# Optimization experiments

Hardware: AMD Instinct MI355X
Metric: run time of the kernel (lower is better)

Reference implementation:

```python
import jax, jax.numpy as jnp
import numpy as np

B, O, GRID = 2048, 48, 112
SIGMA = 5.0


def setup_inputs() -> dict:
    key = jax.random.key(0)
    k1, k2, k3, k4, k5 = jax.random.split(key, 5)
    s = float(GRID - 1)
    xL = jax.random.uniform(k1, (B,), dtype=jnp.float32) * s
    yL = jax.random.uniform(k2, (B,), dtype=jnp.float32) * s
    obj_list = jax.random.uniform(k3, (B, O, 2), dtype=jnp.float32) * s
    obj_num = jax.random.randint(k4, (B,), 0, O + 1, dtype=jnp.int32)
    road_mask = jax.random.randint(k5, (B, GRID, GRID), 0, 2, dtype=jnp.int32)
    return {"xL": xL, "yL": yL, "obj_list": obj_list, "obj_num": obj_num,
            "road_mask": road_mask, "H": GRID, "W": GRID}


def reference(xL, yL, obj_list, obj_num, road_mask, H, W):
    # Faithful vectorization of batch_gaussian_tensor_obj.
    # exp(-(dx^2+dy^2)/(2s^2)) is separable: exp(-dx^2/..) * exp(-dy^2/..),
    # so per-object splats reduce to a batched matmul over the object axis.
    inv = 1.0 / (2.0 * SIGMA * SIGMA)
    x = jnp.arange(H, dtype=jnp.float32)  # row coordinate grid
    y = jnp.arange(W, dtype=jnp.float32)  # col coordinate grid

    # positive goal gaussian, rank-1 outer product per batch element
    gx = jnp.exp(-((x[None, :] - xL[:, None]) ** 2) * inv)  # [B,H]
    gy = jnp.exp(-((y[None, :] - yL[:, None]) ** 2) * inv)  # [B,W]
    goal = gx[:, :, None] * gy[:, None, :]                   # [B,H,W]

    # negative object gaussians; note original swaps xy: xo=xy[1], yo=xy[0]
    xo = obj_list[:, :, 1]  # [B,O] row coords
    yo = obj_list[:, :, 0]  # [B,O] col coords
    ex = jnp.exp(-((x[None, None, :] - xo[:, :, None]) ** 2) * inv)  # [B,O,H]
    ey = jnp.exp(-((y[None, None, :] - yo[:, :, None]) ** 2) * inv)  # [B,O,W]
    valid = (jnp.arange(O)[None, :] < obj_num[:, None]).astype(jnp.float32)  # [B,O]
    obj = jnp.einsum('boh,bow->bhw', ex * valid[:, :, None], ey)     # [B,H,W]

    channel = 0.5 + 0.5 * goal - 0.5 * obj
    channel = jnp.where(road_mask == 0, 0.0, channel)
    return channel
```

## Files before the change

### kernel.cpp

```cpp
#include <hip/hip_runtime.h>

#define GRID_N 112
#define O_MAX 48
#define HW_N (GRID_N * GRID_N)
#define NT 256
#define KPAD 64
#define LSTR 72

typedef _Float16 half8  __attribute__((ext_vector_type(8)));
typedef _Float16 half2v __attribute__((ext_vector_type(2)));
typedef float    f32x4  __attribute__((ext_vector_type(4)));

__global__ __launch_bounds__(NT) void goalmap_kernel(
    const float* __restrict__ xL, const float* __restrict__ yL,
    const float* __restrict__ obj_list, const int* __restrict__ obj_num,
    const int* __restrict__ road_mask, float* __restrict__ out)
{
    constexpr float INV = 1.0f / (2.0f * 5.0f * 5.0f);

    __shared__ _Float16 exT[GRID_N * LSTR];
    __shared__ _Float16 eyT[GRID_N * LSTR];

    const int b   = blockIdx.x;
    const int tid = threadIdx.x;
    const int n   = obj_num[b];
    const float xl = xL[b];
    const float yl = yL[b];
    const float* ob = obj_list + (size_t)b * O_MAX * 2;

    for (int i = tid; i < GRID_N * (KPAD / 2); i += NT) {
        int pos = i >> 5;
        int o0  = (i & 31) * 2;
        half2v vx, vy;
        #pragma unroll
        for (int j = 0; j < 2; ++j) {
            int o = o0 + j;
            float valx = 0.f, valy = 0.f;
            if (o <= n) {
                float cx, cy, s;
                if (o < n) { cx = ob[o * 2 + 1]; cy = ob[o * 2 + 0]; s = -0.5f; }
                else       { cx = xl;            cy = yl;            s =  0.5f; }
                float dx = (float)pos - cx;
                float dy = (float)pos - cy;
                valx = s * __expf(-dx * dx * INV);
                valy =     __expf(-dy * dy * INV);
            }
            vx[j] = (_Float16)valx;
            vy[j] = (_Float16)valy;
        }
        *(half2v*)&exT[pos * LSTR + o0] = vx;
        *(half2v*)&eyT[pos * LSTR + o0] = vy;
    }
    __syncthreads();

    const int* rm = road_mask + (size_t)b * HW_N;
    float*     op = out       + (size_t)b * HW_N;

    const int lane = tid & 63;
    const int wid  = tid >> 6;
    const int m    = lane & 15;
    const int quad = lane >> 4;

    for (int t = wid; t < 49; t += 4) {
        int th = t / 7;
        int tw = t - th * 7;

        const _Float16* arow = &exT[(th * 16 + m) * LSTR + quad * 8];
        const _Float16* brow = &eyT[(tw * 16 + m) * LSTR + quad * 8];
        half8 a0 = *(const half8*)arow;
        half8 b0 = *(const half8*)brow;
        half8 a1 = *(const half8*)(arow + 32);
        half8 b1 = *(const half8*)(brow + 32);

        f32x4 acc = {0.f, 0.f, 0.f, 0.f};
        acc = __builtin_amdgcn_mfma_f32_16x16x32_f16(a0, b0, acc, 0, 0, 0);
        acc = __builtin_amdgcn_mfma_f32_16x16x32_f16(a1, b1, acc, 0, 0, 0);

        int h0 = th * 16 + quad * 4;
        int w0 = tw * 16 + m;
        #pragma unroll
        for (int r = 0; r < 4; ++r) {
            int idx = (h0 + r) * GRID_N + w0;
            int mv = rm[idx];
            float v = 0.5f + acc[r];
            op[idx] = (mv == 0) ? 0.f : v;
        }
    }
}

extern "C" void kernel_launch(void* const* d_in, const int* in_sizes, int n_in,
                              void* d_out, int out_size, void* d_ws, size_t ws_size,
                              hipStream_t stream) {
    const float* xL        = (const float*)d_in[0];
    const float* yL        = (const float*)d_in[1];
    const float* obj_list  = (const float*)d_in[2];
    const int*   obj_num   = (const int*)d_in[3];
    const int*   road_mask = (const int*)d_in[4];
    float*       out       = (float*)d_out;
    const int B = in_sizes[0];

    goalmap_kernel<<<B, NT, 0, stream>>>(xL, yL, obj_list, obj_num, road_mask, out);
}
```

Baseline: 219.6 us.

## Stage MFMA results in LDS and apply mask with vectorized 16-byte loads/stores

```diff
diff --git a/kernel.cpp b/kernel.cpp
--- a/kernel.cpp
+++ b/kernel.cpp
@@ -8,10 +8,11 @@
 #define LSTR 72
 
 typedef _Float16 half8  __attribute__((ext_vector_type(8)));
+typedef _Float16 half4v __attribute__((ext_vector_type(4)));
 typedef _Float16 half2v __attribute__((ext_vector_type(2)));
 typedef float    f32x4  __attribute__((ext_vector_type(4)));
 
-__global__ __launch_bounds__(NT) void goalmap_kernel(
+__global__ __launch_bounds__(NT, 2) void goalmap_kernel(
     const float* __restrict__ xL, const float* __restrict__ yL,
     const float* __restrict__ obj_list, const int* __restrict__ obj_num,
     const int* __restrict__ road_mask, float* __restrict__ out)
@@ -20,6 +21,7 @@
 
     __shared__ _Float16 exT[GRID_N * LSTR];
     __shared__ _Float16 eyT[GRID_N * LSTR];
+    __shared__ _Float16 cmap[HW_N];
 
     const int b   = blockIdx.x;
     const int tid = threadIdx.x;
@@ -53,9 +55,6 @@
     }
     __syncthreads();
 
-    const int* rm = road_mask + (size_t)b * HW_N;
-    float*     op = out       + (size_t)b * HW_N;
-
     const int lane = tid & 63;
     const int wid  = tid >> 6;
     const int m    = lane & 15;
@@ -79,12 +78,43 @@
         int h0 = th * 16 + quad * 4;
         int w0 = tw * 16 + m;
         #pragma unroll
-        for (int r = 0; r < 4; ++r) {
-            int idx = (h0 + r) * GRID_N + w0;
-            int mv = rm[idx];
-            float v = 0.5f + acc[r];
-            op[idx] = (mv == 0) ? 0.f : v;
+        for (int r = 0; r < 4; ++r)
+            cmap[(h0 + r) * GRID_N + w0] = (_Float16)(0.5f + acc[r]);
+    }
+    __syncthreads();
+
+    const int4*  rm4 = (const int4*)(road_mask + (size_t)b * HW_N);
+    float4*      op4 = (float4*)(out + (size_t)b * HW_N);
+
+    #pragma unroll
+    for (int it = 0; it < 3; ++it) {
+        int4   mv[4];
+        half4v cv[4];
+        #pragma unroll
+        for (int j = 0; j < 4; ++j) mv[j] = rm4[(it * 4 + j) * NT + tid];
+        #pragma unroll
+        for (int j = 0; j < 4; ++j)
+            cv[j] = *(const half4v*)&cmap[((it * 4 + j) * NT + tid) * 4];
+        #pragma unroll
+        for (int j = 0; j < 4; ++j) {
+            float4 v;
+            v.x = (mv[j].x == 0) ? 0.f : (float)cv[j][0];
+            v.y = (mv[j].y == 0) ? 0.f : (float)cv[j][1];
+            v.z = (mv[j].z == 0) ? 0.f : (float)cv[j][2];
+            v.w = (mv[j].w == 0) ? 0.f : (float)cv[j][3];
+            op4[(it * 4 + j) * NT + tid] = v;
         }
+    }
+    if (tid < 64) {
+        int idx = 12 * NT + tid;
+        int4   mv = rm4[idx];
+        half4v cv = *(const half4v*)&cmap[idx * 4];
+        float4 v;
+        v.x = (mv.x == 0) ? 0.f : (float)cv[0];
+        v.y = (mv.y == 0) ? 0.f : (float)cv[1];
+        v.z = (mv.z == 0) ? 0.f : (float)cv[2];
+        v.w = (mv.w == 0) ? 0.f : (float)cv[3];
+        op4[idx] = v;
     }
 }
 
```

After: 219.9 us. About the same (+0.1%).

## Prefetch road mask into registers before table build and stage objects in LDS

Applied to the files above, without the earlier changes.

```diff
diff --git a/kernel.cpp b/kernel.cpp
--- a/kernel.cpp
+++ b/kernel.cpp
@@ -18,6 +18,7 @@
 {
     constexpr float INV = 1.0f / (2.0f * 5.0f * 5.0f);
 
+    __shared__ float    obj_s[O_MAX * 2];
     __shared__ _Float16 exT[GRID_N * LSTR];
     __shared__ _Float16 eyT[GRID_N * LSTR];
 
@@ -27,6 +28,31 @@
     const float xl = xL[b];
     const float yl = yL[b];
     const float* ob = obj_list + (size_t)b * O_MAX * 2;
+
+    if (tid < O_MAX * 2) obj_s[tid] = ob[tid];
+
+    const int lane = tid & 63;
+    const int wid  = tid >> 6;
+    const int m    = lane & 15;
+    const int quad = lane >> 4;
+
+    const int* rm = road_mask + (size_t)b * HW_N;
+    float*     op = out       + (size_t)b * HW_N;
+
+    int mpf[13][4];
+    #pragma unroll
+    for (int i = 0; i < 13; ++i) {
+        int t = wid + i * 4;
+        if (t < 49) {
+            int th = t / 7, tw = t - th * 7;
+            int base = (th * 16 + quad * 4) * GRID_N + tw * 16 + m;
+            #pragma unroll
+            for (int r = 0; r < 4; ++r)
+                mpf[i][r] = rm[base + r * GRID_N];
+        }
+    }
+
+    __syncthreads();
 
     for (int i = tid; i < GRID_N * (KPAD / 2); i += NT) {
         int pos = i >> 5;
@@ -38,8 +64,8 @@
             float valx = 0.f, valy = 0.f;
             if (o <= n) {
                 float cx, cy, s;
-                if (o < n) { cx = ob[o * 2 + 1]; cy = ob[o * 2 + 0]; s = -0.5f; }
-                else       { cx = xl;            cy = yl;            s =  0.5f; }
+                if (o < n) { cx = obj_s[o * 2 + 1]; cy = obj_s[o * 2 + 0]; s = -0.5f; }
+                else       { cx = xl;               cy = yl;               s =  0.5f; }
                 float dx = (float)pos - cx;
                 float dy = (float)pos - cy;
                 valx = s * __expf(-dx * dx * INV);
@@ -53,37 +79,30 @@
     }
     __syncthreads();
 
-    const int* rm = road_mask + (size_t)b * HW_N;
-    float*     op = out       + (size_t)b * HW_N;
+    #pragma unroll
+    for (int i = 0; i < 13; ++i) {
+        int t = wid + i * 4;
+        if (t < 49) {
+            int th = t / 7, tw = t - th * 7;
+            const _Float16* arow = &exT[(th * 16 + m) * LSTR + quad * 8];
+            const _Float16* brow = &eyT[(tw * 16 + m) * LSTR + quad * 8];
+            half8 a0 = *(const half8*)arow;
+            half8 b0 = *(const half8*)brow;
+            half8 a1 = *(const half8*)(arow + 32);
+            half8 b1 = *(const half8*)(brow + 32);
 
-    const int lane = tid & 63;
-    const int wid  = tid >> 6;
-    const int m    = lane & 15;
-    const int quad = lane >> 4;
+            f32x4 acc = {0.f, 0.f, 0.f, 0.f};
+            acc = __builtin_amdgcn_mfma_f32_16x16x32_f16(a0, b0, acc, 0, 0, 0);
+            acc = __builtin_amdgcn_mfma_f32_16x16x32_f16(a1, b1, acc, 0, 0, 0);
 
-    for (int t = wid; t < 49; t += 4) {
-        int th = t / 7;
-        int tw = t - th * 7;
-
-        const _Float16* arow = &exT[(th * 16 + m) * LSTR + quad * 8];
-        const _Float16* brow = &eyT[(tw * 16 + m) * LSTR + quad * 8];
-        half8 a0 = *(const half8*)arow;
-        half8 b0 = *(const half8*)brow;
-        half8 a1 = *(const half8*)(arow + 32);
-        half8 b1 = *(const half8*)(brow + 32);
-
-        f32x4 acc = {0.f, 0.f, 0.f, 0.f};
-        acc = __builtin_amdgcn_mfma_f32_16x16x32_f16(a0, b0, acc, 0, 0, 0);
-        acc = __builtin_amdgcn_mfma_f32_16x16x32_f16(a1, b1, acc, 0, 0, 0);
-
-        int h0 = th * 16 + quad * 4;
-        int w0 = tw * 16 + m;
-        #pragma unroll
-        for (int r = 0; r < 4; ++r) {
-            int idx = (h0 + r) * GRID_N + w0;
-            int mv = rm[idx];
-            float v = 0.5f + acc[r];
-            op[idx] = (mv == 0) ? 0.f : v;
+            int h0 = th * 16 + quad * 4;
+            int w0 = tw * 16 + m;
+            #pragma unroll
+            for (int r = 0; r < 4; ++r) {
+                float v = 0.5f + acc[r];
+                v = (mpf[i][r] == 0) ? 0.f : v;
+                __builtin_nontemporal_store(v, &op[(h0 + r) * GRID_N + w0]);
+            }
         }
     }
 }
```

Result: faster. 207.2 us (-5.6%).

## Prefetch road mask before exp build, vectorize stores, skip unused K half

Applied to the files above, without the earlier changes.

```diff
diff --git a/kernel.cpp b/kernel.cpp
--- a/kernel.cpp
+++ b/kernel.cpp
@@ -4,7 +4,6 @@
 #define O_MAX 48
 #define HW_N (GRID_N * GRID_N)
 #define NT 256
-#define KPAD 64
 #define LSTR 72
 
 typedef _Float16 half8  __attribute__((ext_vector_type(8)));
@@ -24,13 +23,37 @@
     const int b   = blockIdx.x;
     const int tid = threadIdx.x;
     const int n   = obj_num[b];
+    const bool k64 = (n >= 32);
     const float xl = xL[b];
     const float yl = yL[b];
     const float* ob = obj_list + (size_t)b * O_MAX * 2;
 
-    for (int i = tid; i < GRID_N * (KPAD / 2); i += NT) {
-        int pos = i >> 5;
-        int o0  = (i & 31) * 2;
+    const int lane = tid & 63;
+    const int wid  = tid >> 6;
+    const int m    = lane & 15;
+    const int quad = lane >> 4;
+
+    const int start = wid * 13;
+    const int cnt   = (wid < 3) ? 13 : 10;
+
+    const int4*   rm4 = (const int4*)(road_mask + (size_t)b * HW_N);
+    float4*       op4 = (float4*)(out + (size_t)b * HW_N);
+
+    int4 mpf[13];
+    #pragma unroll
+    for (int i = 0; i < 13; ++i) {
+        if (i < cnt) {
+            int t  = start + i;
+            int th = t / 7, tw = t - th * 7;
+            mpf[i] = rm4[(th * 16 + m) * 28 + tw * 4 + quad];
+        }
+    }
+
+    const int sh = k64 ? 5 : 4;
+    const int items = GRID_N << sh;
+    for (int i = tid; i < items; i += NT) {
+        int pos = i >> sh;
+        int o0  = (i & ((1 << sh) - 1)) * 2;
         half2v vx, vy;
         #pragma unroll
         for (int j = 0; j < 2; ++j) {
@@ -38,8 +61,12 @@
             float valx = 0.f, valy = 0.f;
             if (o <= n) {
                 float cx, cy, s;
-                if (o < n) { cx = ob[o * 2 + 1]; cy = ob[o * 2 + 0]; s = -0.5f; }
-                else       { cx = xl;            cy = yl;            s =  0.5f; }
+                if (o < n) {
+                    float2 c = *(const float2*)&ob[o * 2];
+                    cx = c.y; cy = c.x; s = -0.5f;
+                } else {
+                    cx = xl; cy = yl; s = 0.5f;
+                }
                 float dx = (float)pos - cx;
                 float dy = (float)pos - cy;
                 valx = s * __expf(-dx * dx * INV);
@@ -53,37 +80,32 @@
     }
     __syncthreads();
 
-    const int* rm = road_mask + (size_t)b * HW_N;
-    float*     op = out       + (size_t)b * HW_N;
+    #pragma unroll
+    for (int i = 0; i < 13; ++i) {
+        if (i < cnt) {
+            int t  = start + i;
+            int th = t / 7, tw = t - th * 7;
 
-    const int lane = tid & 63;
-    const int wid  = tid >> 6;
-    const int m    = lane & 15;
-    const int quad = lane >> 4;
+            const _Float16* arow = &eyT[(tw * 16 + m) * LSTR + quad * 8];
+            const _Float16* brow = &exT[(th * 16 + m) * LSTR + quad * 8];
+            half8 a0 = *(const half8*)arow;
+            half8 b0 = *(const half8*)brow;
 
-    for (int t = wid; t < 49; t += 4) {
-        int th = t / 7;
-        int tw = t - th * 7;
+            f32x4 acc = {0.f, 0.f, 0.f, 0.f};
+            acc = __builtin_amdgcn_mfma_f32_16x16x32_f16(a0, b0, acc, 0, 0, 0);
+            if (k64) {
+                half8 a1 = *(const half8*)(arow + 32);
+                half8 b1 = *(const half8*)(brow + 32);
+                acc = __builtin_amdgcn_mfma_f32_16x16x32_f16(a1, b1, acc, 0, 0, 0);
+            }
 
-        const _Float16* arow = &exT[(th * 16 + m) * LSTR + quad * 8];
-        const _Float16* brow = &eyT[(tw * 16 + m) * LSTR + quad * 8];
-        half8 a0 = *(const half8*)arow;
-        half8 b0 = *(const half8*)brow;
-        half8 a1 = *(const half8*)(arow + 32);
-        half8 b1 = *(const half8*)(brow + 32);
-
-        f32x4 acc = {0.f, 0.f, 0.f, 0.f};
-        acc = __builtin_amdgcn_mfma_f32_16x16x32_f16(a0, b0, acc, 0, 0, 0);
-        acc = __builtin_amdgcn_mfma_f32_16x16x32_f16(a1, b1, acc, 0, 0, 0);
-
-        int h0 = th * 16 + quad * 4;
-        int w0 = tw * 16 + m;
-        #pragma unroll
-        for (int r = 0; r < 4; ++r) {
-            int idx = (h0 + r) * GRID_N + w0;
-            int mv = rm[idx];
-            float v = 0.5f + acc[r];
-            op[idx] = (mv == 0) ? 0.f : v;
+            int4 mv = mpf[i];
+            float4 v;
+            v.x = (mv.x == 0) ? 0.f : 0.5f + acc[0];
+            v.y = (mv.y == 0) ? 0.f : 0.5f + acc[1];
+            v.z = (mv.z == 0) ? 0.f : 0.5f + acc[2];
+            v.w = (mv.w == 0) ? 0.f : 0.5f + acc[3];
+            op4[(th * 16 + m) * 28 + tw * 4 + quad] = v;
         }
     }
 }
```

New measurement: 210.3 us. -4.3%, faster.
